# Kernel tuning notes

Hardware: AMD Instinct MI355X
Metric: run time of the kernel (lower is better)

## Reference

```python
import jax, jax.numpy as jnp
import numpy as np
from jax import lax

EPS = 1e-8  # torch CosineSimilarity eps


def setup_inputs() -> dict:
    key = jax.random.key(0)
    k1, k2, k3 = jax.random.split(key, 3)
    B, T, D, K = 16, 2048, 768, 64
    inputs = jax.random.normal(k1, (B, T, D), dtype=jnp.float32)
    labels = jax.random.randint(k2, (B, T), 0, K, dtype=jnp.int64)
    class_avgs = jax.random.normal(k3, (K, D), dtype=jnp.float32)
    return {"inputs": inputs, "labels": labels, "class_avgs": class_avgs}


def _simrel(inputs, labels, class_avgs):
    B, T, D = inputs.shape
    K = class_avgs.shape[0]
    vecs = inputs.reshape(B * T, D)
    labs = labels.reshape(B * T)
    class_ids = jnp.arange(K)

    def step(carry, xl):
        avgs, counts = carry  # [K,D], [K]
        vec, lab = xl  # [D], scalar int
        is_inf = jnp.any(jnp.isinf(avgs), axis=1)  # [K] unseen-class flag
        vn = jnp.maximum(jnp.linalg.norm(vec), EPS)
        an = jnp.maximum(jnp.linalg.norm(avgs, axis=1), EPS)  # [K]
        cos = (avgs @ vec) / (an * vn)  # [K]
        onehot = class_ids == lab
        # unseen class: sim = 1 (cos(vec,vec)) if labeled, else -1
        sim = jnp.where(is_inf, jnp.where(onehot, 1.0, -1.0), cos)
        # training update: running mean of labeled class (counts reset per forward)
        cnt = counts[lab]
        new_row = jnp.where(is_inf[lab], vec, (avgs[lab] * cnt + vec) / (cnt + 1.0))
        avgs = avgs.at[lab].set(new_row)
        counts = counts.at[lab].add(1.0)
        return (avgs, counts), sim

    init = (class_avgs, jnp.zeros((K,), dtype=inputs.dtype))
    (_, _), sims = lax.scan(step, init, (vecs, labs))
    return sims.reshape(B, T, K)


def reference(inputs, labels, class_avgs):
    return _simrel(inputs, labels, class_avgs)
```

## Files before the change

kernel.cpp:

```cpp
#include <hip/hip_runtime.h>
#include <cstddef>

#define K 64
#define D 768
#define D4 192

__device__ __forceinline__ float d4f(float4 a, float4 b) {
  return a.x*b.x + a.y*b.y + a.z*b.z + a.w*b.w;
}
__device__ __forceinline__ float4 a4(float4 a, float4 b) {
  return make_float4(a.x+b.x, a.y+b.y, a.z+b.z, a.w+b.w);
}
__device__ __forceinline__ unsigned short f2bf(float x) {
  unsigned int u = __float_as_uint(x);
  unsigned int r = (u + 0x7FFFu + ((u >> 16) & 1u)) >> 16;
  return (unsigned short)r;
}
__device__ __forceinline__ float bflo(unsigned u) { return __uint_as_float(u << 16); }
__device__ __forceinline__ float bfhi(unsigned u) { return __uint_as_float(u & 0xFFFF0000u); }

typedef __attribute__((ext_vector_type(8)))  short bf16x8;
typedef __attribute__((ext_vector_type(16))) float f32x16;

#define NCF 256
#define CF  128
#define NF  32768

__global__ __launch_bounds__(256) void k1c(
    const float* __restrict__ cavg, unsigned short* __restrict__ cavgb,
    float* __restrict__ cn2)
{
  int wave = blockIdx.x * 4 + (threadIdx.x >> 6);
  int l = threadIdx.x & 63;
  if (wave >= K) return;
  const float* src = cavg + (size_t)wave * D;
  unsigned short* dst = cavgb + (size_t)wave * D;
  float sq = 0.f;
#pragma unroll
  for (int t = 0; t < 3; ++t) {
    float4 v = ((const float4*)src)[t * 64 + l];
    sq += v.x*v.x + v.y*v.y + v.z*v.z + v.w*v.w;
    ushort4 o; o.x = f2bf(v.x); o.y = f2bf(v.y); o.z = f2bf(v.z); o.w = f2bf(v.w);
    ((ushort4*)dst)[t * 64 + l] = o;
  }
#pragma unroll
  for (int m = 1; m <= 32; m <<= 1) sq += __shfl_xor(sq, m);
  if (l == 0) cn2[wave] = sq;
}

#define LDT2 132
#define LDM  136
__global__ __launch_bounds__(256) void k2_v10(
    const float* __restrict__ inputs, const int* __restrict__ labels,
    unsigned short* __restrict__ sums, int* __restrict__ cnts_t)
{
  __shared__ unsigned short Vt[128 * LDT2];
  __shared__ unsigned short Mt[64 * LDM];
  const int bi = blockIdx.x;
  const int m = bi / 6, g = bi % 6;
  const int tid = threadIdx.x;
  const int w = tid >> 6, l = tid & 63;
  const int r31 = l & 31, kh = l >> 5;

  float4 fa[8], fb[8];
#pragma unroll
  for (int it = 0; it < 8; ++it) {
    int flat = it * 256 + tid;
    int row = flat >> 4, c8 = flat & 15;
    const float* src = inputs + (size_t)(m * 128 + row) * D + g * 128 + c8 * 8;
    fa[it] = *(const float4*)src;
    fb[it] = *(const float4*)(src + 4);
  }

  for (int e = tid; e < 64 * LDM / 2; e += 256) ((unsigned int*)Mt)[e] = 0u;
  __syncthreads();
  if (tid < 128) Mt[labels[m * 128 + tid] * LDM + tid] = 0x3F80;
  __syncthreads();
  if (g == 0 && tid < 64) {
    int c = 0;
    for (int j = 0; j < 128; ++j) c += (Mt[tid * LDM + j] != 0);
    cnts_t[tid * NCF + m] = c;
  }

#pragma unroll
  for (int it = 0; it < 8; ++it) {
    int flat = it * 256 + tid;
    int row = flat >> 4, c8 = flat & 15;
    uint4 u;
    u.x = (unsigned)f2bf(fa[it].x) | ((unsigned)f2bf(fa[it].y) << 16);
    u.y = (unsigned)f2bf(fa[it].z) | ((unsigned)f2bf(fa[it].w) << 16);
    u.z = (unsigned)f2bf(fb[it].x) | ((unsigned)f2bf(fb[it].y) << 16);
    u.w = (unsigned)f2bf(fb[it].z) | ((unsigned)f2bf(fb[it].w) << 16);
    *(uint4*)(Vt + row * LDT2 + c8 * 8) = u;
  }
  __syncthreads();

  f32x16 acc0 = (f32x16){}, acc1 = (f32x16){};
#pragma unroll
  for (int kk = 0; kk < 8; ++kk) {
    bf16x8 a0 = *(const bf16x8*)(Mt + (r31) * LDM + kk * 16 + kh * 8);
    bf16x8 a1 = *(const bf16x8*)(Mt + (32 + r31) * LDM + kk * 16 + kh * 8);
    bf16x8 b;
#pragma unroll
    for (int r = 0; r < 8; ++r)
      b[r] = *(const short*)(Vt + (kk * 16 + kh * 8 + r) * LDT2 + w * 32 + r31);
    acc0 = __builtin_amdgcn_mfma_f32_32x32x16_bf16(a0, b, acc0, 0, 0, 0);
    acc1 = __builtin_amdgcn_mfma_f32_32x32x16_bf16(a1, b, acc1, 0, 0, 0);
  }

  __syncthreads();
  unsigned short* So = Vt;
#pragma unroll
  for (int q = 0; q < 16; ++q) {
    int kc = (q & 3) + 8 * (q >> 2) + 4 * kh;
    So[kc * 128 + w * 32 + r31]        = f2bf(acc0[q]);
    So[(32 + kc) * 128 + w * 32 + r31] = f2bf(acc1[q]);
  }
  __syncthreads();
  unsigned short* sp = sums + (size_t)m * (K * D) + g * 128;
#pragma unroll
  for (int it = 0; it < 4; ++it) {
    int flat = it * 256 + tid;
    int row = flat >> 4, c = flat & 15;
    *(uint4*)(sp + (size_t)row * D + c * 8) = *(const uint4*)(So + row * 128 + c * 8);
  }
}

__global__ __launch_bounds__(256) void k3a_scan_lo(
    unsigned short* __restrict__ sums, float* __restrict__ aux)
{
  const int g  = blockIdx.x / 96;
  const int cp = (blockIdx.x % 96) * 256 + threadIdx.x;
  const int col = cp * 2;
  float run0 = 0.f, run1 = 0.f;
  for (int m = g * 16; m < g * 16 + 16; ++m) {
    size_t idx = (size_t)m * (K * D) + col;
    unsigned u = *(const unsigned*)(sums + idx);
    float t0 = bflo(u), t1 = bfhi(u);
    *(unsigned*)(sums + idx) = (unsigned)f2bf(run0) | ((unsigned)f2bf(run1) << 16);
    run0 += t0; run1 += t1;
  }
  aux[(size_t)g * (K * D) + col]     = run0;
  aux[(size_t)g * (K * D) + col + 1] = run1;
}

__global__ __launch_bounds__(256) void k3b_plus(
    float* __restrict__ aux, int* __restrict__ cnts_t)
{
  if (blockIdx.x == 192) {
    if (threadIdx.x < K) {
      int k = threadIdx.x;
      int run = 0;
      int* p = cnts_t + k * NCF;
      for (int mm = 0; mm < NCF; ++mm) { int t = p[mm]; p[mm] = run; run += t; }
    }
    return;
  }
  int col = blockIdx.x * 256 + threadIdx.x;
  float run = 0.f;
  for (int g = 0; g < 16; ++g) {
    size_t idx = (size_t)g * (K * D) + col;
    float t = aux[idx]; aux[idx] = run; run += t;
  }
}

#define LDV2 136
#define LDD  132
#define BUFW (2 * 128 * LDV2)
__global__ __launch_bounds__(1024, 4) void k4_v8(
    const float* __restrict__ inputs, const unsigned short* __restrict__ base,
    const float* __restrict__ aux, const unsigned short* __restrict__ cavgb,
    const int* __restrict__ labels, const int* __restrict__ cnts_t,
    const float* __restrict__ cn2, float* __restrict__ out)
{
  __shared__ unsigned short smem[2 * BUFW];
  __shared__ float pvL[128];
  __shared__ float bn2L[64];
  __shared__ int   labL[128];
  __shared__ float segA[16][64];
  __shared__ float segF[16][64];
  __shared__ float segP[16][64];
  __shared__ int   segH[16][64];
  const int m = blockIdx.x;
  const int g = m >> 4;
  const int tid = threadIdx.x;
  const int w = tid >> 6, l = tid & 63;
  const int r31 = l & 31, kh = l >> 5;
  const int wr = w & 3;
  const int wc = w >> 2;

  if (tid < 128) labL[tid] = labels[m * 128 + tid];
  if (tid < 64) bn2L[tid] = 0.f;
  __syncthreads();

  f32x16 accP = (f32x16){}, accS = (f32x16){};

  float4 vregf[4];
  uint4 breg, creg;
  float4 areg[2];

#define PREF(sx) do {                                                          \
    _Pragma("unroll")                                                          \
    for (int it = 0; it < 4; ++it) {                                           \
      int flat = it * 1024 + tid;                                              \
      int row = flat >> 5, c4 = flat & 31;                                     \
      vregf[it] = *(const float4*)(inputs + (size_t)(m * 128 + row) * D + (sx) * 128 + c4 * 4); \
    }                                                                          \
    _Pragma("unroll")                                                          \
    for (int it = 0; it < 2; ++it) {                                           \
      int flat = it * 1024 + tid;                                              \
      int row = flat >> 4, c = flat & 15;                                      \
      if (it == 0) {                                                           \
        breg = *(const uint4*)(base + ((size_t)m * K + row) * D + (sx) * 128 + c * 8); \
        const float* ap = aux + ((size_t)g * K + row) * D + (sx) * 128 + c * 8; \
        areg[0] = *(const float4*)ap;                                          \
        areg[1] = *(const float4*)(ap + 4);                                    \
      } else {                                                                 \
        creg = *(const uint4*)(cavgb + (size_t)(row - 64) * D + (sx) * 128 + c * 8); \
      }                                                                        \
    }                                                                          \
  } while (0)

#define WRITEB(pb) do {                                                        \
    unsigned short* Vt_ = smem + (pb) * BUFW;                                  \
    unsigned short* Bt_ = Vt_ + 128 * LDV2;                                    \
    _Pragma("unroll")                                                          \
    for (int it = 0; it < 4; ++it) {                                           \
      int flat = it * 1024 + tid;                                              \
      int row = flat >> 5, c4 = flat & 31;                                     \
      ushort4 o;                                                               \
      o.x = f2bf(vregf[it].x); o.y = f2bf(vregf[it].y);                        \
      o.z = f2bf(vregf[it].z); o.w = f2bf(vregf[it].w);                        \
      *(ushort4*)(Vt_ + row * LDV2 + c4 * 4) = o;                              \
    }                                                                          \
    _Pragma("unroll")                                                          \
    for (int it = 0; it < 2; ++it) {                                           \
      int flat = it * 1024 + tid;                                              \
      int row = flat >> 4, c = flat & 15;                                      \
      if (it == 0) {                                                           \
        uint4 ub = breg;                                                       \
        float4 af0 = areg[0], af1 = areg[1];                                   \
        float f0 = bflo(ub.x) + af0.x, f1 = bfhi(ub.x) + af0.y;                \
        float f2 = bflo(ub.y) + af0.z, f3 = bfhi(ub.y) + af0.w;                \
        float f4 = bflo(ub.z) + af1.x, f5 = bfhi(ub.z) + af1.y;                \
        float f6 = bflo(ub.w) + af1.z, f7 = bfhi(ub.w) + af1.w;                \
        float sq = f0*f0 + f1*f1 + f2*f2 + f3*f3 + f4*f4 + f5*f5 + f6*f6 + f7*f7; \
        sq += __shfl_xor(sq, 1); sq += __shfl_xor(sq, 2);                      \
        sq += __shfl_xor(sq, 4); sq += __shfl_xor(sq, 8);                      \
        if ((l & 15) == 0) atomicAdd(&bn2L[row], sq);                          \
        uint4 u;                                                               \
        u.x = (unsigned)f2bf(f0) | ((unsigned)f2bf(f1) << 16);                 \
        u.y = (unsigned)f2bf(f2) | ((unsigned)f2bf(f3) << 16);                 \
        u.z = (unsigned)f2bf(f4) | ((unsigned)f2bf(f5) << 16);                 \
        u.w = (unsigned)f2bf(f6) | ((unsigned)f2bf(f7) << 16);                 \
        *(uint4*)(Bt_ + row * LDV2 + c * 8) = u;                               \
      } else {                                                                 \
        *(uint4*)(Bt_ + row * LDV2 + c * 8) = creg;                            \
      }                                                                        \
    }                                                                          \
  } while (0)

  PREF(0);
  WRITEB(0);
  PREF(1);
  __syncthreads();

  for (int s = 0; s < 6; ++s) {
    const int pb = s & 1;
    if (s < 5) WRITEB(pb ^ 1);
    if (s < 4) PREF(s + 2);
    const unsigned short* Vt = smem + pb * BUFW;
    const unsigned short* Bt = Vt + 128 * LDV2;
#pragma unroll
    for (int kk = 0; kk < 8; ++kk) {
      bf16x8 av = *(const bf16x8*)(Vt + (32 * wr + r31) * LDV2 + kk * 16 + kh * 8);
      bf16x8 bB = *(const bf16x8*)(Bt + (32 * wc + r31) * LDV2 + kk * 16 + kh * 8);
      accP = __builtin_amdgcn_mfma_f32_32x32x16_bf16(av, bB, accP, 0, 0, 0);
      if (wc <= wr) {
        bf16x8 bV = *(const bf16x8*)(Vt + (32 * wc + r31) * LDV2 + kk * 16 + kh * 8);
        accS = __builtin_amdgcn_mfma_f32_32x32x16_bf16(av, bV, accS, 0, 0, 0);
      }
    }
    __syncthreads();
  }
#undef PREF
#undef WRITEB

  if (wr == wc && ((r31 >> 2) & 1) == kh) {
    int q = (r31 & 3) + 4 * (r31 >> 3);
    pvL[32 * wr + r31] = accS[q];
  }

  {
    unsigned short* Vt = smem;
    unsigned short* Bt = smem + 128 * LDV2;
#pragma unroll
    for (int q = 0; q < 16; ++q) {
      int i = 32 * wr + (q & 3) + 8 * (q >> 2) + 4 * kh;
      int j = 32 * wc + r31;
      Vt[i * LDV2 + j] = (j < i) ? f2bf(accS[q]) : (unsigned short)0;
    }
    int j = tid & 127;
    int lab = labL[j];
    int kb = (tid >> 7) * 8;
#pragma unroll
    for (int kk = 0; kk < 8; ++kk) {
      int k = kb + kk;
      Bt[k * LDV2 + j] = (lab == k) ? (unsigned short)0x3F80 : (unsigned short)0;
    }
  }
  __syncthreads();

  if (w < 8) {
    const unsigned short* Vt = smem;
    const unsigned short* Bt = smem + 128 * LDV2;
#pragma unroll
    for (int kk = 0; kk < 8; ++kk) {
      bf16x8 aS = *(const bf16x8*)(Vt + (32 * wr + r31) * LDV2 + kk * 16 + kh * 8);
      bf16x8 bM = *(const bf16x8*)(Bt + (32 * wc + r31) * LDV2 + kk * 16 + kh * 8);
      accP = __builtin_amdgcn_mfma_f32_32x32x16_bf16(aS, bM, accP, 0, 0, 0);
    }
  }
  __syncthreads();

  float* dotL = (float*)smem;
#pragma unroll
  for (int q = 0; q < 16; ++q) {
    int i = 32 * wr + (q & 3) + 8 * (q >> 2) + 4 * kh;
    dotL[i * LDD + 32 * wc + r31] = accP[q];
  }
  __syncthreads();

  {
    int k = l;
    float A = 0.f, Fv = 0.f, Pv = 0.f;
    int has = 0;
    int jb = w * 8;
    for (int j = jb; j < jb + 8; ++j) {
      if (labL[j] == k) {
        float t = 2.f * dotL[j * LDD + k] + pvL[j];
        A += t;
        if (!has) { Fv = t; Pv = pvL[j]; has = 1; }
      }
    }
    segA[w][k] = A; segF[w][k] = Fv; segP[w][k] = Pv; segH[w][k] = has;
  }
  __syncthreads();

  {
    int k = l;
    bool seen = cnts_t[k * NCF + m] > 0;
    float n = seen ? bn2L[k] : 0.f;
    for (int ww = 0; ww < w; ++ww) {
      if (segH[ww][k]) {
        n = seen ? (n + segA[ww][k])
                 : (segP[ww][k] + segA[ww][k] - segF[ww][k]);
        seen = true;
      }
    }
    float cnk = cn2[k];
    int jb = w * 8;
    for (int j = jb; j < jb + 8; ++j) {
      float dS = dotL[j * LDD + k];
      float dC = dotL[j * LDD + 64 + k];
      float pvj = pvL[j];
      int lab = labL[j];
      float val = seen ? dS : dC;
      float nn  = seen ? n : cnk;
      out[(size_t)(m * 128 + j) * K + k] = val * rsqrtf(fmaxf(nn * pvj, 1e-30f));
      if (lab == k) {
        n = seen ? (n + 2.f * dS + pvj) : pvj;
        seen = true;
      }
    }
  }
}

__global__ __launch_bounds__(256) void ph1_chunk_sums(
    const float* __restrict__ inputs, const int* __restrict__ labels,
    float* __restrict__ sums, int* __restrict__ cnts, int NC, int C)
{
  __shared__ float acc[4 * K * 64];
  __shared__ int   hist[4 * K];
  const int bi    = blockIdx.x;
  const int chunk = bi / 12, slice = bi % 12;
  const int w = threadIdx.x >> 6, l = threadIdx.x & 63;

  for (int e = threadIdx.x; e < 4 * K * 64; e += 256) acc[e] = 0.f;
  hist[threadIdx.x] = 0;
  __syncthreads();

  const int C4 = C >> 2;
  const long long rbase = (long long)chunk * C + (long long)w * C4;
  float* accw = acc + w * (K * 64);
  for (int j = 0; j < C4; ++j) {
    long long r = rbase + j;
    int lab = labels[r];
    float v = inputs[r * D + slice * 64 + l];
    accw[lab * 64 + l] += v;
    if (slice == 0 && l == 0) hist[w * K + lab]++;
  }
  __syncthreads();

  float* sp = sums + (long long)chunk * (K * D) + slice * 64;
  for (int e = threadIdx.x; e < K * 64; e += 256) {
    int k = e >> 6, dl = e & 63;
    float s = acc[0*K*64 + e] + acc[1*K*64 + e] + acc[2*K*64 + e] + acc[3*K*64 + e];
    sp[k * D + dl] = s;
  }
  if (slice == 0 && threadIdx.x < K) {
    cnts[chunk * K + threadIdx.x] =
        hist[0*K + threadIdx.x] + hist[1*K + threadIdx.x] +
        hist[2*K + threadIdx.x] + hist[3*K + threadIdx.x];
  }
}

__global__ __launch_bounds__(256) void ph2a_scan_sums(float* __restrict__ sums, int NC)
{
  const int tid = blockIdx.x * 256 + threadIdx.x;
  float run = 0.f;
  for (int m = 0; m < NC; ++m) {
    long long idx = (long long)m * (K * D) + tid;
    float t = sums[idx];
    sums[idx] = run;
    run += t;
  }
}

__global__ void ph2b_scan_cnts(int* __restrict__ cnts, int NC)
{
  const int k = threadIdx.x;
  int run = 0;
  for (int m = 0; m < NC; ++m) {
    int t = cnts[m * K + k];
    cnts[m * K + k] = run;
    run += t;
  }
}

__global__ __launch_bounds__(256, 4) void ph3_scan(
    const float* __restrict__ inputs, const int* __restrict__ labels,
    const float* __restrict__ cavg, const float* __restrict__ base,
    const int* __restrict__ cnts, float* __restrict__ out, int NC, int C)
{
  const int bi = blockIdx.x;
  int chunk, quad;
  if (NC >= 8) {
    int xcd = bi & 7, slot = bi >> 3;
    chunk = xcd * (NC >> 3) + (slot >> 2);
    quad  = slot & 3;
  } else {
    chunk = bi >> 2; quad = bi & 3;
  }
  const int w = threadIdx.x >> 6, l = threadIdx.x & 63;
  const int k0 = (quad * 4 + w) * 4;

  const int cb = chunk * K + k0;
  bool vg0 = (cnts[cb+0] == 0), vg1 = (cnts[cb+1] == 0);
  bool vg2 = (cnts[cb+2] == 0), vg3 = (cnts[cb+3] == 0);

  const float4* bp = (const float4*)base + (long long)chunk * (K * D4);
  const float4* cp = (const float4*)cavg;

  float4 A0[3], A1[3], A2[3], A3[3];
#pragma unroll
  for (int t = 0; t < 3; ++t) {
    int o = t * 64 + l;
    A0[t] = vg0 ? cp[(k0+0)*D4 + o] : bp[(k0+0)*D4 + o];
    A1[t] = vg1 ? cp[(k0+1)*D4 + o] : bp[(k0+1)*D4 + o];
    A2[t] = vg2 ? cp[(k0+2)*D4 + o] : bp[(k0+2)*D4 + o];
    A3[t] = vg3 ? cp[(k0+3)*D4 + o] : bp[(k0+3)*D4 + o];
  }
  float n0 = 0.f, n1 = 0.f, n2 = 0.f, n3 = 0.f;
#pragma unroll
  for (int t = 0; t < 3; ++t) {
    n0 += d4f(A0[t], A0[t]); n1 += d4f(A1[t], A1[t]);
    n2 += d4f(A2[t], A2[t]); n3 += d4f(A3[t], A3[t]);
  }
#pragma unroll
  for (int m = 1; m <= 32; m <<= 1) {
    n0 += __shfl_xor(n0, m); n1 += __shfl_xor(n1, m);
    n2 += __shfl_xor(n2, m); n3 += __shfl_xor(n3, m);
  }

  const long long ibase = (long long)chunk * C;
  for (int j = 0; j < C; ++j) {
    const long long i = ibase + j;
    const int lab = labels[i];
    const float4* vp = (const float4*)inputs + i * D4;
    float4 v0 = vp[l], v1 = vp[64 + l], v2 = vp[128 + l];

    float p0 = d4f(A0[0], v0) + d4f(A0[1], v1) + d4f(A0[2], v2);
    float p1 = d4f(A1[0], v0) + d4f(A1[1], v1) + d4f(A1[2], v2);
    float p2 = d4f(A2[0], v0) + d4f(A2[1], v1) + d4f(A2[2], v2);
    float p3 = d4f(A3[0], v0) + d4f(A3[1], v1) + d4f(A3[2], v2);
    float pv = d4f(v0, v0) + d4f(v1, v1) + d4f(v2, v2);
#pragma unroll
    for (int m = 1; m <= 32; m <<= 1) {
      p0 += __shfl_xor(p0, m); p1 += __shfl_xor(p1, m);
      p2 += __shfl_xor(p2, m); p3 += __shfl_xor(p3, m);
      pv += __shfl_xor(pv, m);
    }
    if (l < 4) {
      float ps = (l == 0) ? p0 : (l == 1) ? p1 : (l == 2) ? p2 : p3;
      float ns = (l == 0) ? n0 : (l == 1) ? n1 : (l == 2) ? n2 : n3;
      out[i * K + k0 + l] = ps * rsqrtf(fmaxf(ns * pv, 1e-30f));
    }
#define UPD(idx) do { \
      if (vg##idx) { A##idx[0]=v0; A##idx[1]=v1; A##idx[2]=v2; n##idx = pv; vg##idx = false; } \
      else { A##idx[0]=a4(A##idx[0],v0); A##idx[1]=a4(A##idx[1],v1); A##idx[2]=a4(A##idx[2],v2); \
             n##idx += 2.f * p##idx + pv; } } while (0)
    if      (lab == k0 + 0) UPD(0);
    else if (lab == k0 + 1) UPD(1);
    else if (lab == k0 + 2) UPD(2);
    else if (lab == k0 + 3) UPD(3);
#undef UPD
  }
}

extern "C" void kernel_launch(void* const* d_in, const int* in_sizes, int n_in,
                              void* d_out, int out_size, void* d_ws, size_t ws_size,
                              hipStream_t stream)
{
  const float* inputs = (const float*)d_in[0];
  const int*   labels = (const int*)d_in[1];
  const float* cavg   = (const float*)d_in[2];
  float* out = (float*)d_out;
  const int N = in_sizes[1];

  const size_t szSums  = (size_t)NCF * K * D * 2;
  const size_t szAux   = (size_t)16 * K * D * 4;
  const size_t szCnt   = (size_t)K * NCF * 4;
  const size_t szCavgb = (size_t)K * D * 2;
  const size_t szCn2   = (size_t)K * 4;
  size_t need = szSums + szAux + szCnt + szCavgb + szCn2 + 8 * 256;

  if (N == NF && in_sizes[2] == K * D && ws_size >= need) {
    char* p = (char*)d_ws;
    auto take = [&](size_t b) { char* r = p; p += (b + 255) & ~(size_t)255; return r; };
    unsigned short* sums  = (unsigned short*)take(szSums);
    float*          aux   = (float*)take(szAux);
    int*            cnts  = (int*)take(szCnt);
    unsigned short* cavgb = (unsigned short*)take(szCavgb);
    float*          cn2   = (float*)take(szCn2);

    hipLaunchKernelGGL(k1c, dim3(16), dim3(256), 0, stream, cavg, cavgb, cn2);
    hipLaunchKernelGGL(k2_v10, dim3(NCF * 6), dim3(256), 0, stream,
                       inputs, labels, sums, cnts);
    hipLaunchKernelGGL(k3a_scan_lo, dim3(16 * 96), dim3(256), 0, stream, sums, aux);
    hipLaunchKernelGGL(k3b_plus, dim3(193), dim3(256), 0, stream, aux, cnts);
    hipLaunchKernelGGL(k4_v8, dim3(NCF), dim3(1024), 0, stream,
                       inputs, sums, aux, cavgb, labels, cnts, cn2, out);
    return;
  }

  int NC = 256;
  while (NC > 1) {
    size_t nd = (size_t)NC * K * D * 4 + (size_t)NC * K * 4;
    if (nd <= ws_size && (N % (NC * 4)) == 0) break;
    NC >>= 1;
  }
  const int C = N / NC;
  float* d_sums = (float*)d_ws;
  int*   d_cnts = (int*)((char*)d_ws + (size_t)NC * K * D * 4);

  hipLaunchKernelGGL(ph1_chunk_sums, dim3(NC * 12), dim3(256), 0, stream,
                     inputs, labels, d_sums, d_cnts, NC, C);
  hipLaunchKernelGGL(ph2a_scan_sums, dim3((K * D) / 256), dim3(256), 0, stream,
                     d_sums, NC);
  hipLaunchKernelGGL(ph2b_scan_cnts, dim3(1), dim3(64), 0, stream,
                     d_cnts, NC);
  hipLaunchKernelGGL(ph3_scan, dim3(NC * 4), dim3(256), 0, stream,
                     inputs, labels, cavg, d_sums, d_cnts, out, NC, C);
}
```

Baseline: 78.79 us.

## Fuse class-avg conversion into chunk-sum kernel and halve column tile per block

Merges the small class-average bf16 conversion/norm kernel into the chunk-sum kernel as extra trailing blocks, removing one launch. The chunk-sum kernel now splits D into 12 column groups of 64 instead of 6 of 128, doubling the block count and halving per-block registers and LDS, with each wave doing one MFMA chain instead of two. Per-chunk label counts now come from a shared-memory atomic histogram rather than a serial scan of the one-hot matrix. More blocks may improve occupancy and latency hiding, at the cost of redundant one-hot matrix construction per block and narrower global loads.

```diff
diff --git a/kernel.cpp b/kernel.cpp
--- a/kernel.cpp
+++ b/kernel.cpp
@@ -26,86 +26,85 @@
 #define CF  128
 #define NF  32768
 
-__global__ __launch_bounds__(256) void k1c(
+#define LDT3 68
+#define LDM  136
+__global__ __launch_bounds__(256) void k2_v11(
+    const float* __restrict__ inputs, const int* __restrict__ labels,
     const float* __restrict__ cavg, unsigned short* __restrict__ cavgb,
-    float* __restrict__ cn2)
-{
-  int wave = blockIdx.x * 4 + (threadIdx.x >> 6);
-  int l = threadIdx.x & 63;
-  if (wave >= K) return;
-  const float* src = cavg + (size_t)wave * D;
-  unsigned short* dst = cavgb + (size_t)wave * D;
-  float sq = 0.f;
-#pragma unroll
-  for (int t = 0; t < 3; ++t) {
-    float4 v = ((const float4*)src)[t * 64 + l];
-    sq += v.x*v.x + v.y*v.y + v.z*v.z + v.w*v.w;
-    ushort4 o; o.x = f2bf(v.x); o.y = f2bf(v.y); o.z = f2bf(v.z); o.w = f2bf(v.w);
-    ((ushort4*)dst)[t * 64 + l] = o;
-  }
-#pragma unroll
-  for (int m = 1; m <= 32; m <<= 1) sq += __shfl_xor(sq, m);
-  if (l == 0) cn2[wave] = sq;
-}
-
-#define LDT2 132
-#define LDM  136
-__global__ __launch_bounds__(256) void k2_v10(
-    const float* __restrict__ inputs, const int* __restrict__ labels,
+    float* __restrict__ cn2,
     unsigned short* __restrict__ sums, int* __restrict__ cnts_t)
 {
-  __shared__ unsigned short Vt[128 * LDT2];
+  __shared__ unsigned short Vt[128 * LDT3];
   __shared__ unsigned short Mt[64 * LDM];
+  __shared__ int hist[64];
   const int bi = blockIdx.x;
-  const int m = bi / 6, g = bi % 6;
   const int tid = threadIdx.x;
+
+  if (bi >= NCF * 12) {
+    int wave = (bi - NCF * 12) * 4 + (tid >> 6);
+    int l = tid & 63;
+    if (wave >= K) return;
+    const float* src = cavg + (size_t)wave * D;
+    unsigned short* dst = cavgb + (size_t)wave * D;
+    float sq = 0.f;
+#pragma unroll
+    for (int t = 0; t < 3; ++t) {
+      float4 v = ((const float4*)src)[t * 64 + l];
+      sq += v.x*v.x + v.y*v.y + v.z*v.z + v.w*v.w;
+      ushort4 o; o.x = f2bf(v.x); o.y = f2bf(v.y); o.z = f2bf(v.z); o.w = f2bf(v.w);
+      ((ushort4*)dst)[t * 64 + l] = o;
+    }
+#pragma unroll
+    for (int mm = 1; mm <= 32; mm <<= 1) sq += __shfl_xor(sq, mm);
+    if (l == 0) cn2[wave] = sq;
+    return;
+  }
+
+  const int m = bi / 12, g = bi % 12;
   const int w = tid >> 6, l = tid & 63;
   const int r31 = l & 31, kh = l >> 5;
-
-  float4 fa[8], fb[8];
+  const int ch = w & 1;
+  const int cw = w >> 1;
+
+  float4 fr[8];
 #pragma unroll
   for (int it = 0; it < 8; ++it) {
     int flat = it * 256 + tid;
-    int row = flat >> 4, c8 = flat & 15;
-    const float* src = inputs + (size_t)(m * 128 + row) * D + g * 128 + c8 * 8;
-    fa[it] = *(const float4*)src;
-    fb[it] = *(const float4*)(src + 4);
+    int row = flat >> 4, c4 = flat & 15;
+    fr[it] = *(const float4*)(inputs + (size_t)(m * 128 + row) * D + g * 64 + c4 * 4);
   }
 
   for (int e = tid; e < 64 * LDM / 2; e += 256) ((unsigned int*)Mt)[e] = 0u;
-  __syncthreads();
-  if (tid < 128) Mt[labels[m * 128 + tid] * LDM + tid] = 0x3F80;
-  __syncthreads();
-  if (g == 0 && tid < 64) {
-    int c = 0;
-    for (int j = 0; j < 128; ++j) c += (Mt[tid * LDM + j] != 0);
-    cnts_t[tid * NCF + m] = c;
-  }
+  if (tid < 64) hist[tid] = 0;
+  __syncthreads();
+  if (tid < 128) {
+    int lab = labels[m * 128 + tid];
+    Mt[lab * LDM + tid] = 0x3F80;
+    if (g == 0) atomicAdd(&hist[lab], 1);
+  }
+  __syncthreads();
+  if (g == 0 && tid < 64) cnts_t[tid * NCF + m] = hist[tid];
 
 #pragma unroll
   for (int it = 0; it < 8; ++it) {
     int flat = it * 256 + tid;
-    int row = flat >> 4, c8 = flat & 15;
-    uint4 u;
-    u.x = (unsigned)f2bf(fa[it].x) | ((unsigned)f2bf(fa[it].y) << 16);
-    u.y = (unsigned)f2bf(fa[it].z) | ((unsigned)f2bf(fa[it].w) << 16);
-    u.z = (unsigned)f2bf(fb[it].x) | ((unsigned)f2bf(fb[it].y) << 16);
-    u.w = (unsigned)f2bf(fb[it].z) | ((unsigned)f2bf(fb[it].w) << 16);
-    *(uint4*)(Vt + row * LDT2 + c8 * 8) = u;
-  }
-  __syncthreads();
-
-  f32x16 acc0 = (f32x16){}, acc1 = (f32x16){};
+    int row = flat >> 4, c4 = flat & 15;
+    ushort4 o;
+    o.x = f2bf(fr[it].x); o.y = f2bf(fr[it].y);
+    o.z = f2bf(fr[it].z); o.w = f2bf(fr[it].w);
+    *(ushort4*)(Vt + row * LDT3 + c4 * 4) = o;
+  }
+  __syncthreads();
+
+  f32x16 acc = (f32x16){};
 #pragma unroll
   for (int kk = 0; kk < 8; ++kk) {
-    bf16x8 a0 = *(const bf16x8*)(Mt + (r31) * LDM + kk * 16 + kh * 8);
-    bf16x8 a1 = *(const bf16x8*)(Mt + (32 + r31) * LDM + kk * 16 + kh * 8);
+    bf16x8 a = *(const bf16x8*)(Mt + (ch * 32 + r31) * LDM + kk * 16 + kh * 8);
     bf16x8 b;
 #pragma unroll
     for (int r = 0; r < 8; ++r)
-      b[r] = *(const short*)(Vt + (kk * 16 + kh * 8 + r) * LDT2 + w * 32 + r31);
-    acc0 = __builtin_amdgcn_mfma_f32_32x32x16_bf16(a0, b, acc0, 0, 0, 0);
-    acc1 = __builtin_amdgcn_mfma_f32_32x32x16_bf16(a1, b, acc1, 0, 0, 0);
+      b[r] = *(const short*)(Vt + (kk * 16 + kh * 8 + r) * LDT3 + cw * 32 + r31);
+    acc = __builtin_amdgcn_mfma_f32_32x32x16_bf16(a, b, acc, 0, 0, 0);
   }
 
   __syncthreads();
@@ -113,16 +112,15 @@
 #pragma unroll
   for (int q = 0; q < 16; ++q) {
     int kc = (q & 3) + 8 * (q >> 2) + 4 * kh;
-    So[kc * 128 + w * 32 + r31]        = f2bf(acc0[q]);
-    So[(32 + kc) * 128 + w * 32 + r31] = f2bf(acc1[q]);
-  }
-  __syncthreads();
-  unsigned short* sp = sums + (size_t)m * (K * D) + g * 128;
-#pragma unroll
-  for (int it = 0; it < 4; ++it) {
+    So[(ch * 32 + kc) * 64 + cw * 32 + r31] = f2bf(acc[q]);
+  }
+  __syncthreads();
+  unsigned short* sp = sums + (size_t)m * (K * D) + g * 64;
+#pragma unroll
+  for (int it = 0; it < 2; ++it) {
     int flat = it * 256 + tid;
-    int row = flat >> 4, c = flat & 15;
-    *(uint4*)(sp + (size_t)row * D + c * 8) = *(const uint4*)(So + row * 128 + c * 8);
+    int row = flat >> 3, c = flat & 7;
+    *(uint4*)(sp + (size_t)row * D + c * 8) = *(const uint4*)(So + row * 64 + c * 8);
   }
 }
 
@@ -544,9 +542,8 @@
     unsigned short* cavgb = (unsigned short*)take(szCavgb);
     float*          cn2   = (float*)take(szCn2);
 
-    hipLaunchKernelGGL(k1c, dim3(16), dim3(256), 0, stream, cavg, cavgb, cn2);
-    hipLaunchKernelGGL(k2_v10, dim3(NCF * 6), dim3(256), 0, stream,
-                       inputs, labels, sums, cnts);
+    hipLaunchKernelGGL(k2_v11, dim3(NCF * 12 + 16), dim3(256), 0, stream,
+                       inputs, labels, cavg, cavgb, cn2, sums, cnts);
     hipLaunchKernelGGL(k3a_scan_lo, dim3(16 * 96), dim3(256), 0, stream, sums, aux);
     hipLaunchKernelGGL(k3b_plus, dim3(193), dim3(256), 0, stream, aux, cnts);
     hipLaunchKernelGGL(k4_v8, dim3(NCF), dim3(1024), 0, stream,
```

Result: faster. 72.71 us, median of 2 (-7.7%).
